# Performance work log

Hardware: AMD Instinct MI355X
Metric: run time of the kernel (lower is better)

Reference implementation:

```python
import jax, jax.numpy as jnp
import numpy as np

B, T, C = 1, 4096, 1024
N_HEAD = 16
HEAD_DIM = C // N_HEAD
SCALE = 1.0 / np.sqrt(HEAD_DIM).astype(np.float32)


def setup_inputs() -> dict:
    key = jax.random.key(0)
    k1, k2, k3 = jax.random.split(key, 3)
    x = jax.random.normal(k1, (B, T, C), dtype=jnp.float32)
    W_attn = jax.random.normal(k2, (C, 3 * C), dtype=jnp.float32) * 0.02
    b_attn = jnp.zeros((3 * C,), dtype=jnp.float32)
    W_proj = jax.random.normal(k3, (C, C), dtype=jnp.float32) * 0.02
    b_proj = jnp.zeros((C,), dtype=jnp.float32)
    return {"x": x, "W_attn": W_attn, "b_attn": b_attn, "W_proj": W_proj, "b_proj": b_proj}


def reference(x, W_attn, b_attn, W_proj, b_proj):
    Bq, Tq, Cq = x.shape
    qkv = x @ W_attn + b_attn                      # [B, T, 3C]
    q, k, v = jnp.split(qkv, 3, axis=-1)
    # split heads -> [B, H, T, D]
    def split_heads(t):
        return t.reshape(Bq, Tq, N_HEAD, HEAD_DIM).transpose(0, 2, 1, 3)
    q, k, v = split_heads(q), split_heads(k), split_heads(v)
    scores = jnp.einsum('bhqd,bhkd->bhqk', q, k) * SCALE  # [B, H, T, T]
    causal = jnp.tril(jnp.ones((Tq, Tq), dtype=bool))
    scores = jnp.where(causal[None, None], scores, jnp.float32(-jnp.inf))
    probs = jax.nn.softmax(scores, axis=-1)
    out = jnp.einsum('bhqk,bhkd->bhqd', probs, v)          # [B, H, T, D]
    out = out.transpose(0, 2, 1, 3).reshape(Bq, Tq, Cq)    # merge heads
    out = out @ W_proj + b_proj
    return out
```

## Files before the change

kernel.cpp:

```cpp
#include <hip/hip_runtime.h>
#include <hip/hip_bf16.h>


typedef unsigned short u16;
typedef u16 u16x4 __attribute__((ext_vector_type(4)));
typedef u16 u16x8 __attribute__((ext_vector_type(8)));
typedef __bf16 bf16x8 __attribute__((ext_vector_type(8)));
typedef float f32x4 __attribute__((ext_vector_type(4)));

#define T_SEQ 4096
#define C_DIM 1024
#define NH 16
#define HD 64
#define QSC 0.18033688f
#define NJOBS 1152

static __device__ __forceinline__ u16 f2bf(float f) {
    __hip_bfloat16 h = __float2bfloat16(f);
    return __builtin_bit_cast(u16, h);
}

static __device__ __forceinline__ float bf2f(u16 u) {
    return __builtin_bit_cast(float, (unsigned)u << 16);
}

static __device__ __forceinline__ bf16x8 ldfr(const u16* base, int byteoff) {
    return __builtin_bit_cast(bf16x8, *(const u16x8*)(base + (byteoff >> 1)));
}

static __device__ __forceinline__ void gld_lds16(const void* g, void* l) {
    __builtin_amdgcn_global_load_lds((const __attribute__((address_space(1))) void*)g,
                                     (__attribute__((address_space(3))) void*)l, 16, 0, 0);
}

#define MFMA16(a, b, c) __builtin_amdgcn_mfma_f32_16x16x32_bf16((a), (b), (c), 0, 0, 0)


__global__ __launch_bounds__(256) void k_prep(const float* __restrict__ x, u16* __restrict__ xb,
                                              const float* __restrict__ W_attn, u16* __restrict__ Wat,
                                              const float* __restrict__ W_proj, u16* __restrict__ Wpt,
                                              unsigned* __restrict__ cnt) {
    const int b = blockIdx.x;
    const int tid = threadIdx.x;
    if (b == 0 && tid == 0) *cnt = 0u;

    if (b < 2048) {
        const int i = (b * 256 + tid) * 8;
        float4 a = *(const float4*)(x + i);
        float4 c = *(const float4*)(x + i + 4);
        u16x8 o;
        o[0] = f2bf(a.x); o[1] = f2bf(a.y); o[2] = f2bf(a.z); o[3] = f2bf(a.w);
        o[4] = f2bf(c.x); o[5] = f2bf(c.y); o[6] = f2bf(c.z); o[7] = f2bf(c.w);
        *(u16x8*)(xb + i) = o;
        return;
    }
    const float* src;
    u16* dst;
    int bx, by, R, Cc;
    if (b < 5120) {
        const int t = b - 2048;
        bx = (t % 96) * 32; by = (t / 96) * 32;
        src = W_attn; dst = Wat; R = 1024; Cc = 3072;
    } else {
        const int t = b - 5120;
        bx = (t & 31) * 32; by = (t >> 5) * 32;
        src = W_proj; dst = Wpt; R = 1024; Cc = 1024;
    }
    __shared__ float tile[32][33];
    const int xi = tid & 31, yi = tid >> 5;
#pragma unroll
    for (int i = 0; i < 32; i += 8)
        tile[yi + i][xi] = src[(size_t)(by + yi + i) * Cc + bx + xi];
    __syncthreads();
#pragma unroll
    for (int i = 0; i < 32; i += 8)
        dst[(size_t)(bx + yi + i) * R + by + xi] = f2bf(tile[xi][yi + i]);
}


template <int EPI>
__global__ __launch_bounds__(256) void k_gemm(const u16* __restrict__ A, const u16* __restrict__ Bt,
                                              const float* __restrict__ bias,
                                              u16* __restrict__ outQ, u16* __restrict__ outK,
                                              u16* __restrict__ outVt, float* __restrict__ outF,
                                              int kd, int nbx) {
    __shared__ u16 Al[128 * 64];
    __shared__ u16 Bl[128 * 64];
    const int tid = threadIdx.x;
    const int lane = tid & 63;
    const int wid = tid >> 6;
    const int wm = wid >> 1, wn = wid & 1;
    const int c = lane & 15, g = lane >> 4;
    const int nwg = gridDim.x;
    const int swzb = ((int)blockIdx.x & 7) * (nwg >> 3) + ((int)blockIdx.x >> 3);
    const int m0 = (swzb % nbx) * 128;
    const int n0 = (swzb / nbx) * 128;
    const int srow = lane >> 3;
    const int sxu = (((lane & 7) * 16) ^ (srow << 4)) >> 1;
    const int swa = (c & 7) << 4;

    f32x4 acc[4][4] = {};

    for (int k0 = 0; k0 < kd; k0 += 64) {
#pragma unroll
        for (int i = 0; i < 4; ++i) {
            const int ch = wid * 4 + i;
            const int row = ch * 8 + srow;
            gld_lds16(A + (size_t)(m0 + row) * kd + k0 + sxu, &Al[ch * 512]);
            gld_lds16(Bt + (size_t)(n0 + row) * kd + k0 + sxu, &Bl[ch * 512]);
        }
        __syncthreads();
        bf16x8 af[4][2], bfm[4][2];
#pragma unroll
        for (int mi = 0; mi < 4; ++mi) {
            const u16* p = Al + (wm * 64 + mi * 16 + c) * 64;
            af[mi][0] = ldfr(p, (16 * g) ^ swa);
            af[mi][1] = ldfr(p, (64 + 16 * g) ^ swa);
        }
#pragma unroll
        for (int ni = 0; ni < 4; ++ni) {
            const u16* p = Bl + (wn * 64 + ni * 16 + c) * 64;
            bfm[ni][0] = ldfr(p, (16 * g) ^ swa);
            bfm[ni][1] = ldfr(p, (64 + 16 * g) ^ swa);
        }
#pragma unroll
        for (int mi = 0; mi < 4; ++mi)
#pragma unroll
            for (int ni = 0; ni < 4; ++ni) {
                acc[mi][ni] = MFMA16(af[mi][0], bfm[ni][0], acc[mi][ni]);
                acc[mi][ni] = MFMA16(af[mi][1], bfm[ni][1], acc[mi][ni]);
            }
        __syncthreads();
    }

    const int mbase = m0 + wm * 64;
    const int nbase = n0 + wn * 64;
    if (EPI == 0) {
        const int part = m0 >> 10;
#pragma unroll
        for (int mi = 0; mi < 4; ++mi) {
            const int fbase = mbase + mi * 16 + 4 * g;
            const f32x4 bv = *(const f32x4*)(bias + fbase);
            const int fr = fbase & 1023;
            const int h = fr >> 6, d0 = fr & 63;
#pragma unroll
            for (int ni = 0; ni < 4; ++ni) {
                const int tok = nbase + ni * 16 + c;
                if (part == 2) {
#pragma unroll
                    for (int r = 0; r < 4; ++r)
                        outVt[(size_t)(fr + r) * T_SEQ + tok] = f2bf(acc[mi][ni][r] + bv[r]);
                } else {
                    u16x4 pk;
#pragma unroll
                    for (int r = 0; r < 4; ++r) {
                        float v = acc[mi][ni][r] + bv[r];
                        pk[r] = f2bf(part == 0 ? v * QSC : v);
                    }
                    u16* dst = (part == 0 ? outQ : outK);
                    *(u16x4*)(dst + (size_t)(h * T_SEQ + tok) * HD + d0) = pk;
                }
            }
        }
    } else {
#pragma unroll
        for (int mi = 0; mi < 4; ++mi) {
            const int fbase = mbase + mi * 16 + 4 * g;
            const f32x4 bv = *(const f32x4*)(bias + fbase);
#pragma unroll
            for (int ni = 0; ni < 4; ++ni) {
                const int tok = nbase + ni * 16 + c;
                f32x4 w;
#pragma unroll
                for (int r = 0; r < 4; ++r) w[r] = acc[mi][ni][r] + bv[r];
                *(f32x4*)(outF + (size_t)tok * C_DIM + fbase) = w;
            }
        }
    }
}


static __device__ __forceinline__ void p_gen(f32x4 s[4], int qabs, int kv0, int g,
                                             bool domask, bf16x8 pa[2]) {
    if (domask) {
#pragma unroll
        for (int tau = 0; tau < 4; ++tau) {
            const int kb = kv0 + 32 * (tau >> 1) + 4 * (tau & 1) + 8 * g;
#pragma unroll
            for (int r = 0; r < 4; ++r)
                if (kb + r > qabs) s[tau][r] = -3e38f;
        }
    }
    u16 pb[4][4];
#pragma unroll
    for (int tau = 0; tau < 4; ++tau)
#pragma unroll
        for (int r = 0; r < 4; ++r)
            pb[tau][r] = f2bf(__builtin_amdgcn_exp2f(s[tau][r]));
    const u16x8 p0 = {pb[0][0], pb[0][1], pb[0][2], pb[0][3], pb[1][0], pb[1][1], pb[1][2], pb[1][3]};
    const u16x8 p1 = {pb[2][0], pb[2][1], pb[2][2], pb[2][3], pb[3][0], pb[3][1], pb[3][2], pb[3][3]};
    pa[0] = __builtin_bit_cast(bf16x8, p0);
    pa[1] = __builtin_bit_cast(bf16x8, p1);
}

__global__ __launch_bounds__(512, 4) void k_flash(const u16* __restrict__ Qg, const u16* __restrict__ Kg,
                                                  const u16* __restrict__ Vtg, u16* __restrict__ Ab,
                                                  u16* __restrict__ part, float* __restrict__ lpart,
                                                  unsigned* __restrict__ cnt) {
    __shared__ u16 sm[3][2][4096];
    __shared__ unsigned jslot;

    const int tid = threadIdx.x;
    const int lane = tid & 63;
    const int wid = tid >> 6;
    const int c = lane & 15, g = lane >> 4;
    const int srow = lane >> 3;
    const int sxu = (((lane & 7) * 16) ^ (srow << 4)) >> 1;

    const u16x8 onespat = {0x3F80, 0x3F80, 0x3F80, 0x3F80, 0x3F80, 0x3F80, 0x3F80, 0x3F80};
    const bf16x8 onesf = __builtin_bit_cast(bf16x8, onespat);

    for (;;) {
        if (tid == 0) jslot = atomicAdd(cnt, 1u);
        __syncthreads();
        const unsigned j = jslot;
        if (j >= (unsigned)NJOBS) break;

        const int head = (int)(j & 15u);
        const int idx = (int)(j >> 4);
        int qb, ch, nc;
        if (idx < 16)      { qb = 15 - (idx >> 3); ch = idx & 7; nc = 8; }
        else if (idx < 30) { const int t = idx - 16; qb = 13 - t / 7;    ch = t % 7; nc = 7; }
        else if (idx < 42) { const int t = idx - 30; qb = 11 - t / 6;    ch = t % 6; nc = 6; }
        else if (idx < 52) { const int t = idx - 42; qb = 9 - t / 5;     ch = t % 5; nc = 5; }
        else if (idx < 60) { const int t = idx - 52; qb = 7 - (t >> 2);  ch = t & 3; nc = 4; }
        else if (idx < 66) { const int t = idx - 60; qb = 5 - t / 3;     ch = t % 3; nc = 3; }
        else if (idx < 70) { const int t = idx - 66; qb = 3 - (t >> 1);  ch = t & 1; nc = 2; }
        else               { qb = 1 - (idx - 70); ch = 0; nc = 1; }
        const int ntile = 4 * qb + 4;
        const int cbase = ntile / nc, crem = ntile % nc;
        const int len = cbase + (ch < crem ? 1 : 0);
        const int start = ch * cbase + (ch < crem ? ch : crem);

        const int q0w = qb * 256 + wid * 32;

        const u16* Qh = Qg + (size_t)head * (T_SEQ * HD);
        const u16* Kh = Kg + (size_t)head * (T_SEQ * HD);
        const u16* Vh = Vtg + (size_t)head * (HD * T_SEQ);

        bf16x8 qf[2][2];
#pragma unroll
        for (int h = 0; h < 2; ++h)
#pragma unroll
            for (int dc = 0; dc < 2; ++dc)
                qf[h][dc] = __builtin_bit_cast(
                    bf16x8, *(const u16x8*)(Qh + (q0w + 16 * h + c) * HD + dc * 32 + 8 * g));

        f32x4 o0[4] = {}, o1[4] = {}, ol0 = {}, ol1 = {};

#pragma unroll
        for (int i = 0; i < 2; ++i) {
            const int ts = (i < len ? start + i : start + len - 1) * 64;
            gld_lds16(Kh + (ts + wid * 8 + srow) * HD + sxu, &sm[i][0][wid * 512]);
            gld_lds16(Vh + (wid * 8 + srow) * T_SEQ + ts + sxu, &sm[i][1][wid * 512]);
        }

        int cur = 0;
        for (int t = 0; t < len; ++t) {
            asm volatile("s_waitcnt vmcnt(2)" ::: "memory");
            __builtin_amdgcn_s_barrier();
            __builtin_amdgcn_sched_barrier(0);
            {
                const int ts = (t + 2 < len ? start + t + 2 : start + len - 1) * 64;
                const int sl = (cur == 0) ? 2 : cur - 1;
                gld_lds16(Kh + (ts + wid * 8 + srow) * HD + sxu, &sm[sl][0][wid * 512]);
                gld_lds16(Vh + (wid * 8 + srow) * T_SEQ + ts + sxu, &sm[sl][1][wid * 512]);
            }
            const int kv0 = (start + t) * 64;
            if (kv0 <= q0w + 31) {
                const u16* Kl = &sm[cur][0][0];
                const u16* Vl = &sm[cur][1][0];
                f32x4 s0[4], s1[4];
                __builtin_amdgcn_s_setprio(1);
#pragma unroll
                for (int tau = 0; tau < 4; ++tau) {
                    const int prow = 32 * (tau >> 1) + 4 * (tau & 1) + 8 * (c >> 2) + (c & 3);
                    const int sw = (prow & 7) << 4;
                    const u16* kb = Kl + prow * 64;
                    const bf16x8 k0 = ldfr(kb, (16 * g) ^ sw);
                    const bf16x8 k1 = ldfr(kb, (64 + 16 * g) ^ sw);
                    f32x4 z0 = {}, z1 = {};
                    z0 = MFMA16(k0, qf[0][0], z0);
                    s0[tau] = MFMA16(k1, qf[0][1], z0);
                    z1 = MFMA16(k0, qf[1][0], z1);
                    s1[tau] = MFMA16(k1, qf[1][1], z1);
                }
                __builtin_amdgcn_s_setprio(0);
                const bool dm0 = (kv0 + 63) > (q0w);
                const bool dm1 = (kv0 + 63) > (q0w + 16);
                bf16x8 pa0[2], pa1[2];
                p_gen(s0, q0w + c, kv0, g, dm0, pa0);
                p_gen(s1, q0w + 16 + c, kv0, g, dm1, pa1);
                const int swv = (c & 7) << 4;
                __builtin_amdgcn_s_setprio(1);
#pragma unroll
                for (int n = 0; n < 4; ++n) {
                    const u16* vb = Vl + (n * 16 + c) * 64;
                    const bf16x8 v0 = ldfr(vb, (16 * g) ^ swv);
                    const bf16x8 v1 = ldfr(vb, (64 + 16 * g) ^ swv);
                    o0[n] = MFMA16(v0, pa0[0], o0[n]);
                    o0[n] = MFMA16(v1, pa0[1], o0[n]);
                    o1[n] = MFMA16(v0, pa1[0], o1[n]);
                    o1[n] = MFMA16(v1, pa1[1], o1[n]);
                }
                ol0 = MFMA16(onesf, pa0[0], ol0);
                ol0 = MFMA16(onesf, pa0[1], ol0);
                ol1 = MFMA16(onesf, pa1[0], ol1);
                ol1 = MFMA16(onesf, pa1[1], ol1);
                __builtin_amdgcn_s_setprio(0);
            }
            cur = (cur == 2) ? 0 : cur + 1;
        }

        const int ql0 = wid * 32 + c;
        if (nc == 1) {
            const float li0 = 1.0f / ol0[0], li1 = 1.0f / ol1[0];
            u16* dst0 = Ab + (size_t)(qb * 256 + ql0) * C_DIM + head * HD;
            u16* dst1 = dst0 + (size_t)16 * C_DIM;
#pragma unroll
            for (int n = 0; n < 4; ++n) {
                u16x4 w0, w1;
#pragma unroll
                for (int r = 0; r < 4; ++r) {
                    w0[r] = f2bf(o0[n][r] * li0);
                    w1[r] = f2bf(o1[n][r] * li1);
                }
                *(u16x4*)(dst0 + n * 16 + 4 * g) = w0;
                *(u16x4*)(dst1 + n * 16 + 4 * g) = w1;
            }
        } else {
            u16* slot = part + (size_t)j * 16384u;
            float* lsl = lpart + (size_t)j * 256u;
#pragma unroll
            for (int n = 0; n < 4; ++n) {
                u16x4 w0, w1;
#pragma unroll
                for (int r = 0; r < 4; ++r) {
                    w0[r] = f2bf(o0[n][r]);
                    w1[r] = f2bf(o1[n][r]);
                }
                *(u16x4*)(slot + ql0 * 64 + n * 16 + 4 * g) = w0;
                *(u16x4*)(slot + (ql0 + 16) * 64 + n * 16 + 4 * g) = w1;
            }
            if (g == 0) {
                lsl[ql0] = ol0[0];
                lsl[ql0 + 16] = ol1[0];
            }
        }
        __syncthreads();
    }
}


__global__ __launch_bounds__(512) void k_combine(const u16* __restrict__ part,
                                                 const float* __restrict__ lpart,
                                                 u16* __restrict__ Ab) {
    const int head = blockIdx.x / 14;
    const int qb = 2 + (blockIdx.x % 14);
    int nc, idx0;
    if (qb >= 14)      { nc = 8; idx0 = (15 - qb) * 8; }
    else if (qb >= 12) { nc = 7; idx0 = 16 + (13 - qb) * 7; }
    else if (qb >= 10) { nc = 6; idx0 = 30 + (11 - qb) * 6; }
    else if (qb >= 8)  { nc = 5; idx0 = 42 + (9 - qb) * 5; }
    else if (qb >= 6)  { nc = 4; idx0 = 52 + (7 - qb) * 4; }
    else if (qb >= 4)  { nc = 3; idx0 = 60 + (5 - qb) * 3; }
    else               { nc = 2; idx0 = 66 + (3 - qb) * 2; }

    const int q = threadIdx.x >> 1;
    const int dh = (threadIdx.x & 1) * 32;
    float acc[32] = {};
    float l = 0.f;
    for (int i = 0; i < nc; ++i) {
        const unsigned jj = (unsigned)(((idx0 + i) << 4) | head);
        const u16* sp = part + (size_t)jj * 16384u + q * 64 + dh;
#pragma unroll
        for (int v = 0; v < 4; ++v) {
            const u16x8 w = *(const u16x8*)(sp + 8 * v);
#pragma unroll
            for (int e = 0; e < 8; ++e) acc[8 * v + e] += bf2f(w[e]);
        }
        l += lpart[(size_t)jj * 256u + q];
    }
    const float li = 1.0f / l;
    u16* dst = Ab + (size_t)(qb * 256 + q) * C_DIM + head * HD + dh;
#pragma unroll
    for (int v = 0; v < 4; ++v) {
        u16x8 w;
#pragma unroll
        for (int e = 0; e < 8; ++e) w[e] = f2bf(acc[8 * v + e] * li);
        *(u16x8*)(dst + 8 * v) = w;
    }
}


extern "C" void kernel_launch(void* const* d_in, const int* in_sizes, int n_in,
                              void* d_out, int out_size, void* d_ws, size_t ws_size,
                              hipStream_t stream) {
    const float* x      = (const float*)d_in[0];
    const float* W_attn = (const float*)d_in[1];
    const float* b_attn = (const float*)d_in[2];
    const float* W_proj = (const float*)d_in[3];
    const float* b_proj = (const float*)d_in[4];
    float* out = (float*)d_out;

    char* ws = (char*)d_ws;
    u16* xb    = (u16*)(ws);
    u16* Wat   = (u16*)(ws + (8u << 20));
    u16* Wpt   = (u16*)(ws + (14u << 20));
    u16* Qb    = (u16*)(ws + (16u << 20));
    u16* Kb    = (u16*)(ws + (24u << 20));
    u16* Vtb   = (u16*)(ws + (32u << 20));
    u16* prt   = (u16*)(ws + (40u << 20));
    float* lpt = (float*)(ws + (78u << 20));
    u16* Ab    = xb;

    unsigned* cnt = (unsigned*)d_out;

    k_prep<<<6144, 256, 0, stream>>>(x, xb, W_attn, Wat, W_proj, Wpt, cnt);
    k_gemm<0><<<768, 256, 0, stream>>>(Wat, xb, b_attn, Qb, Kb, Vtb, nullptr, 1024, 24);
    k_flash<<<768, 512, 0, stream>>>(Qb, Kb, Vtb, Ab, prt, lpt, cnt);
    k_combine<<<224, 512, 0, stream>>>(prt, lpt, Ab);
    k_gemm<1><<<256, 256, 0, stream>>>(Wpt, Ab, b_proj, nullptr, nullptr, nullptr, out, 1024, 8);
}
```

Before: 146.5 us.

## Double-buffer GEMM LDS loads with 512-thread 128x256 tiles

Rewrites the GEMM kernel to use 8 waves and a 128x256 output tile per block, with two LDS stages so global->LDS loads for step t+2 overlap the MFMA work on step t. It swaps the XOR-swizzled layout for a fragment-ordered LDS layout, uses vmcnt waits plus raw barriers in place of __syncthreads, and raises wave priority around the MFMA block. The aim is to hide load latency and cut barrier stalls. In exchange it uses more LDS (96KB) and launches half as many blocks, which lowers grid parallelism, especially for the 128-block projection GEMM.

```diff
diff --git a/kernel.cpp b/kernel.cpp
--- a/kernel.cpp
+++ b/kernel.cpp
@@ -26,6 +26,10 @@
 
 static __device__ __forceinline__ bf16x8 ldfr(const u16* base, int byteoff) {
     return __builtin_bit_cast(bf16x8, *(const u16x8*)(base + (byteoff >> 1)));
+}
+
+static __device__ __forceinline__ bf16x8 ldc(const u16* p) {
+    return __builtin_bit_cast(bf16x8, *(const u16x8*)p);
 }
 
 static __device__ __forceinline__ void gld_lds16(const void* g, void* l) {
@@ -79,50 +83,69 @@
 
 
 template <int EPI>
-__global__ __launch_bounds__(256) void k_gemm(const u16* __restrict__ A, const u16* __restrict__ Bt,
+__global__ __launch_bounds__(512) void k_gemm(const u16* __restrict__ A, const u16* __restrict__ Bt,
                                               const float* __restrict__ bias,
                                               u16* __restrict__ outQ, u16* __restrict__ outK,
                                               u16* __restrict__ outVt, float* __restrict__ outF,
                                               int kd, int nbx) {
-    __shared__ u16 Al[128 * 64];
-    __shared__ u16 Bl[128 * 64];
+    __shared__ u16 Asm[2][8192];
+    __shared__ u16 Bsm[2][16384];
     const int tid = threadIdx.x;
     const int lane = tid & 63;
     const int wid = tid >> 6;
-    const int wm = wid >> 1, wn = wid & 1;
+    const int wm = wid >> 2;
+    const int wn = wid & 3;
     const int c = lane & 15, g = lane >> 4;
     const int nwg = gridDim.x;
     const int swzb = ((int)blockIdx.x & 7) * (nwg >> 3) + ((int)blockIdx.x >> 3);
     const int m0 = (swzb % nbx) * 128;
-    const int n0 = (swzb / nbx) * 128;
-    const int srow = lane >> 3;
-    const int sxu = (((lane & 7) * 16) ^ (srow << 4)) >> 1;
-    const int swa = (c & 7) << 4;
+    const int n0 = (swzb / nbx) * 256;
+    const int srow = lane & 15;
+    const int scol = (lane >> 4) * 8;
 
     f32x4 acc[4][4] = {};
-
-    for (int k0 = 0; k0 < kd; k0 += 64) {
-#pragma unroll
-        for (int i = 0; i < 4; ++i) {
-            const int ch = wid * 4 + i;
-            const int row = ch * 8 + srow;
-            gld_lds16(A + (size_t)(m0 + row) * kd + k0 + sxu, &Al[ch * 512]);
-            gld_lds16(Bt + (size_t)(n0 + row) * kd + k0 + sxu, &Bl[ch * 512]);
-        }
-        __syncthreads();
+    const int nk = kd >> 6;
+
+    auto stage = [&](int s, int sl) {
+        const int k0 = s * 64;
+#pragma unroll
+        for (int kh = 0; kh < 2; ++kh)
+            gld_lds16(A + (size_t)(m0 + wid * 16 + srow) * kd + k0 + kh * 32 + scol,
+                      &Asm[sl][wid * 1024 + kh * 512]);
+#pragma unroll
+        for (int i = 0; i < 2; ++i) {
+            const int rb = wid + i * 8;
+#pragma unroll
+            for (int kh = 0; kh < 2; ++kh)
+                gld_lds16(Bt + (size_t)(n0 + rb * 16 + srow) * kd + k0 + kh * 32 + scol,
+                          &Bsm[sl][rb * 1024 + kh * 512]);
+        }
+    };
+
+    stage(0, 0);
+    stage(1, 1);
+
+    for (int t = 0; t < nk; ++t) {
+        asm volatile("s_waitcnt vmcnt(6)" ::: "memory");
+        __builtin_amdgcn_s_barrier();
+        __builtin_amdgcn_sched_barrier(0);
+
+        const u16* Asl = Asm[t & 1];
+        const u16* Bsl = Bsm[t & 1];
         bf16x8 af[4][2], bfm[4][2];
 #pragma unroll
         for (int mi = 0; mi < 4; ++mi) {
-            const u16* p = Al + (wm * 64 + mi * 16 + c) * 64;
-            af[mi][0] = ldfr(p, (16 * g) ^ swa);
-            af[mi][1] = ldfr(p, (64 + 16 * g) ^ swa);
+            const u16* p = Asl + (wm * 4 + mi) * 1024 + g * 128 + c * 8;
+            af[mi][0] = ldc(p);
+            af[mi][1] = ldc(p + 512);
         }
 #pragma unroll
         for (int ni = 0; ni < 4; ++ni) {
-            const u16* p = Bl + (wn * 64 + ni * 16 + c) * 64;
-            bfm[ni][0] = ldfr(p, (16 * g) ^ swa);
-            bfm[ni][1] = ldfr(p, (64 + 16 * g) ^ swa);
-        }
+            const u16* p = Bsl + (wn * 4 + ni) * 1024 + g * 128 + c * 8;
+            bfm[ni][0] = ldc(p);
+            bfm[ni][1] = ldc(p + 512);
+        }
+        __builtin_amdgcn_s_setprio(1);
 #pragma unroll
         for (int mi = 0; mi < 4; ++mi)
 #pragma unroll
@@ -130,8 +153,13 @@
                 acc[mi][ni] = MFMA16(af[mi][0], bfm[ni][0], acc[mi][ni]);
                 acc[mi][ni] = MFMA16(af[mi][1], bfm[ni][1], acc[mi][ni]);
             }
-        __syncthreads();
-    }
+        __builtin_amdgcn_s_setprio(0);
+        __builtin_amdgcn_sched_barrier(0);
+        __builtin_amdgcn_s_barrier();
+        __builtin_amdgcn_sched_barrier(0);
+        stage(t + 2 < nk ? t + 2 : nk - 1, t & 1);
+    }
+    asm volatile("s_waitcnt vmcnt(0)" ::: "memory");
 
     const int mbase = m0 + wm * 64;
     const int nbase = n0 + wn * 64;
@@ -427,8 +455,8 @@
     unsigned* cnt = (unsigned*)d_out;
 
     k_prep<<<6144, 256, 0, stream>>>(x, xb, W_attn, Wat, W_proj, Wpt, cnt);
-    k_gemm<0><<<768, 256, 0, stream>>>(Wat, xb, b_attn, Qb, Kb, Vtb, nullptr, 1024, 24);
+    k_gemm<0><<<384, 512, 0, stream>>>(Wat, xb, b_attn, Qb, Kb, Vtb, nullptr, 1024, 24);
     k_flash<<<768, 512, 0, stream>>>(Qb, Kb, Vtb, Ab, prt, lpt, cnt);
     k_combine<<<224, 512, 0, stream>>>(prt, lpt, Ab);
-    k_gemm<1><<<256, 256, 0, stream>>>(Wpt, Ab, b_proj, nullptr, nullptr, nullptr, out, 1024, 8);
-}
+    k_gemm<1><<<128, 512, 0, stream>>>(Wpt, Ab, b_proj, nullptr, nullptr, nullptr, out, 1024, 8);
+}
```

Measured after the change: 204.7 us. +39.8%, slower.
